# Kernel tuning notes

Measured on AMD Instinct MI355X. Metric: run time of the kernel, lower is better.

## Reference

```python
import jax, jax.numpy as jnp
import numpy as np


def setup_inputs() -> dict:
    key = jax.random.key(0)
    k1, k2, k3, k4, k5 = jax.random.split(key, 5)
    return {
        "d1": jax.random.normal(k1, (2, 4096, 512), dtype=jnp.float32),
        "d2": jax.random.normal(k2, (2, 512, 4096), dtype=jnp.float32),
        "d3": jax.random.normal(k3, (2, 4096, 512), dtype=jnp.float32),
        "d4": jax.random.normal(k4, (512, 512), dtype=jnp.float32),
        "d5": jax.random.normal(k5, (1, 512), dtype=jnp.float32),
    }


def reference(d1, d2, d3, d4, d5):
    # attention core: scores = d1 @ d2 -> [2, 4096, 4096]
    scores = jnp.einsum('bsd,bdt->bst', d1, d2)
    attn = jax.nn.softmax(scores, axis=2)
    # weighted values: [2, 4096, 512]
    ctx = jnp.einsum('bst,btd->bsd', attn, d3)
    # flatten batch*seq and apply final projection with bias (addmm)
    x = ctx.reshape(8192, 512)
    return d5 + x @ d4  # d5 [1,512] broadcasts over rows
```

## Files before the change

### kernel.cpp

```cpp
#include <hip/hip_runtime.h>

typedef unsigned short u16;
typedef __attribute__((ext_vector_type(8))) short short8;
typedef __attribute__((ext_vector_type(4))) float f32x4;

#define MFMA16(a, b, c) __builtin_amdgcn_mfma_f32_16x16x32_bf16((a), (b), (c), 0, 0, 0)

constexpr int Bb = 2, Ss = 4096, Tt = 4096, Dd = 512;
constexpr int BM = 64, BN = 64, TP = 4;
constexpr int TPART = Tt / TP;
constexpr int TCH = TPART / BN;

constexpr size_t SZ_BF = (size_t)Bb * Ss * Dd * 2;
constexpr size_t O_QH  = 0;
constexpr size_t O_QL  = O_QH + SZ_BF;
constexpr size_t O_D2TH = O_QL + SZ_BF;
constexpr size_t O_D2TL = O_D2TH + SZ_BF;
constexpr size_t O_D3T  = O_D2TL + SZ_BF;
constexpr size_t O_D4T  = O_D3T + SZ_BF;
constexpr size_t O_CTX  = O_D4T + (size_t)512 * 512 * 2;
constexpr size_t O_OP   = O_CTX + SZ_BF;
constexpr size_t O_MP   = O_OP + (size_t)TP * SZ_BF;
constexpr size_t O_LP   = O_MP + (size_t)TP * Bb * Ss * 4;

__device__ __forceinline__ u16 f2bf(float x) {
  union { float f; unsigned u; } v; v.f = x;
  unsigned r = v.u + 0x7fffu + ((v.u >> 16) & 1u);
  return (u16)(r >> 16);
}
__device__ __forceinline__ float bf2f(u16 h) {
  union { unsigned u; float f; } v; v.u = ((unsigned)h) << 16;
  return v.f;
}

__device__ __forceinline__ void gl_lds16(const u16* g, u16* l) {
  __builtin_amdgcn_global_load_lds((const __attribute__((address_space(1))) void*)g,
                                   (__attribute__((address_space(3))) void*)l, 16, 0, 0);
}

__global__ void cvt_split_kernel(const float* __restrict__ in,
                                 u16* __restrict__ outh, u16* __restrict__ outl) {
  const int i = blockIdx.x * 256 + threadIdx.x;
  float4 v = ((const float4*)in)[i];
  ushort4 hh, ll;
  hh.x = f2bf(v.x); ll.x = f2bf(v.x - bf2f(hh.x));
  hh.y = f2bf(v.y); ll.y = f2bf(v.y - bf2f(hh.y));
  hh.z = f2bf(v.z); ll.z = f2bf(v.z - bf2f(hh.z));
  hh.w = f2bf(v.w); ll.w = f2bf(v.w - bf2f(hh.w));
  ((ushort4*)outh)[i] = hh;
  ((ushort4*)outl)[i] = ll;
}

__global__ void transpose_split_kernel(const float* __restrict__ in,
                                       u16* __restrict__ outh,
                                       u16* __restrict__ outl,
                                       int R, int C) {
  __shared__ float tile[32][33];
  int b = blockIdx.z;
  const float* inb = in + (size_t)b * R * C;
  int x = blockIdx.x * 32 + threadIdx.x;
  int y0 = blockIdx.y * 32;
  for (int j = threadIdx.y; j < 32; j += 8)
    tile[j][threadIdx.x] = inb[(size_t)(y0 + j) * C + x];
  __syncthreads();
  size_t ob = (size_t)b * C * R;
  for (int j = threadIdx.y; j < 32; j += 8) {
    float v = tile[threadIdx.x][j];
    size_t oi = ob + (size_t)(blockIdx.x * 32 + j) * R + (y0 + threadIdx.x);
    u16 h = f2bf(v);
    outh[oi] = h;
    if (outl) outl[oi] = f2bf(v - bf2f(h));
  }
}

__global__ __launch_bounds__(256, 3)
void flash_part_kernel(const u16* __restrict__ qh_g,
                       const u16* __restrict__ ql_g,
                       const u16* __restrict__ d2th,
                       const u16* __restrict__ d2tl,
                       const u16* __restrict__ d3t,
                       u16* __restrict__ opart,
                       float* __restrict__ mpart,
                       float* __restrict__ lpart) {
  __shared__ __align__(1024) u16 sbuf[2][8192];
  __shared__ __align__(16) u16 ph[64 * 72];

  const int tid = threadIdx.x;
  const int wave = tid >> 6, lane = tid & 63, quad = lane >> 4, l15 = lane & 15;
  const int m0 = wave * 16;
  const int s0 = blockIdx.x * BM, tp = blockIdx.y, b = blockIdx.z;
  const int rr = lane >> 3, sl = lane & 7;
  const int x7 = l15 & 7;

  f32x4 o_acc[32];
#pragma unroll
  for (int i = 0; i < 32; i++) o_acc[i] = (f32x4){0.f, 0.f, 0.f, 0.f};
  float m_r[4] = {-INFINITY, -INFINITY, -INFINITY, -INFINITY};
  float l_r[4] = {0.f, 0.f, 0.f, 0.f};

  const u16* qh_row = qh_g + ((size_t)b * Ss + s0 + m0 + l15) * Dd + quad * 8;
  const u16* ql_row = ql_g + ((size_t)b * Ss + s0 + m0 + l15) * Dd + quad * 8;
  const u16* kh_b = d2th + (size_t)b * Tt * Dd;
  const u16* kl_b = d2tl + (size_t)b * Tt * Dd;
  const u16* v_b  = d3t  + (size_t)b * Dd * Tt;

  short8 qh_r[16], ql_r[16];
#pragma unroll
  for (int t = 0; t < 16; t++) {
    qh_r[t] = *(const short8*)(qh_row + t * 32);
    ql_r[t] = *(const short8*)(ql_row + t * 32);
  }

  auto issueK = [&](int t0, int d0, int bp) {
#pragma unroll
    for (int i = 0; i < 2; i++) {
      const int r0 = wave * 16 + i * 8;
      const int r = r0 + rr;
      const size_t so = (size_t)(t0 + r) * Dd + d0 + ((sl ^ rr) << 3);
      gl_lds16(kh_b + so, &sbuf[bp][r0 * 64]);
      gl_lds16(kl_b + so, &sbuf[bp][4096 + r0 * 64]);
    }
  };
  auto issueV = [&](int t0, int nc, int bp) {
#pragma unroll
    for (int i = 0; i < 4; i++) {
      const int r0 = wave * 32 + i * 8;
      const int r = r0 + rr;
      gl_lds16(v_b + (size_t)(nc * 128 + r) * Tt + t0 + ((sl ^ rr) << 3),
               &sbuf[bp][r0 * 64]);
    }
  };

  issueK(tp * TPART, 0, 0);
  __syncthreads();

  for (int tc = 0; tc < TCH; tc++) {
    const int t0 = tp * TPART + tc * BN;
    f32x4 s_acc[4];
#pragma unroll
    for (int nt = 0; nt < 4; nt++) s_acc[nt] = (f32x4){0.f, 0.f, 0.f, 0.f};

#pragma unroll
    for (int u = 0; u < 8; u++) {
      if (u < 7) issueK(t0, (u + 1) * 64, (u + 1) & 1);
      else       issueV(t0, 0, (u + 1) & 1);
      __builtin_amdgcn_s_setprio(1);
#pragma unroll
      for (int ks = 0; ks < 2; ks++) {
        const int t = u * 2 + ks;
        const int g = ks * 4 + quad;
#pragma unroll
        for (int nt = 0; nt < 4; nt++) {
          const int off = (nt * 16 + l15) * 64 + ((g ^ x7) << 3);
          short8 bh = *(const short8*)&sbuf[u & 1][off];
          short8 bl = *(const short8*)&sbuf[u & 1][4096 + off];
          s_acc[nt] = MFMA16(qh_r[t], bh, s_acc[nt]);
          s_acc[nt] = MFMA16(ql_r[t], bh, s_acc[nt]);
          s_acc[nt] = MFMA16(qh_r[t], bl, s_acc[nt]);
        }
      }
      __builtin_amdgcn_s_setprio(0);
      __syncthreads();
    }

    float alpha[4], psum[4];
#pragma unroll
    for (int r = 0; r < 4; r++) {
      float v = fmaxf(fmaxf(s_acc[0][r], s_acc[1][r]), fmaxf(s_acc[2][r], s_acc[3][r]));
      v = fmaxf(v, __shfl_xor(v, 1));
      v = fmaxf(v, __shfl_xor(v, 2));
      v = fmaxf(v, __shfl_xor(v, 4));
      v = fmaxf(v, __shfl_xor(v, 8));
      float mn = fmaxf(m_r[r], v);
      alpha[r] = __expf(m_r[r] - mn);
      m_r[r] = mn;
      psum[r] = 0.f;
    }
#pragma unroll
    for (int nt = 0; nt < 4; nt++) {
#pragma unroll
      for (int r = 0; r < 4; r++) {
        float p = __expf(s_acc[nt][r] - m_r[r]);
        psum[r] += p;
        ph[(m0 + quad * 4 + r) * 72 + nt * 16 + l15] = f2bf(p);
      }
    }
#pragma unroll
    for (int r = 0; r < 4; r++) {
      float v = psum[r];
      v += __shfl_xor(v, 1);
      v += __shfl_xor(v, 2);
      v += __shfl_xor(v, 4);
      v += __shfl_xor(v, 8);
      l_r[r] = l_r[r] * alpha[r] + v;
    }
#pragma unroll
    for (int j = 0; j < 32; j++) {
#pragma unroll
      for (int r = 0; r < 4; r++) o_acc[j][r] *= alpha[r];
    }

#pragma unroll
    for (int nc = 0; nc < 4; nc++) {
      const int u = 8 + nc;
      if (nc < 3) issueV(t0, nc + 1, (u + 1) & 1);
      else {
        const int tcn = (tc + 1 < TCH) ? tc + 1 : 0;
        issueK(tp * TPART + tcn * BN, 0, (u + 1) & 1);
      }
      __builtin_amdgcn_s_setprio(1);
#pragma unroll
      for (int ks = 0; ks < 2; ks++) {
        const int kk = ks * 32 + quad * 8;
        const int g = ks * 4 + quad;
        short8 ap = *(const short8*)&ph[(m0 + l15) * 72 + kk];
#pragma unroll
        for (int nt = 0; nt < 8; nt++) {
          const int off = (nt * 16 + l15) * 64 + ((g ^ x7) << 3);
          short8 bv = *(const short8*)&sbuf[u & 1][off];
          o_acc[nc * 8 + nt] = MFMA16(ap, bv, o_acc[nc * 8 + nt]);
        }
      }
      __builtin_amdgcn_s_setprio(0);
      __syncthreads();
    }
  }

  const size_t obase = (((size_t)tp * Bb + b) * Ss + s0) * Dd;
#pragma unroll
  for (int j = 0; j < 32; j++) {
    const int col = (j >> 3) * 128 + (j & 7) * 16 + l15;
#pragma unroll
    for (int r = 0; r < 4; r++) {
      const int row = m0 + quad * 4 + r;
      opart[obase + (size_t)row * Dd + col] = f2bf(o_acc[j][r]);
    }
  }
  if (l15 == 0) {
    const size_t sbase = ((size_t)tp * Bb + b) * Ss + s0;
#pragma unroll
    for (int r = 0; r < 4; r++) {
      const int row = m0 + quad * 4 + r;
      mpart[sbase + row] = m_r[r];
      lpart[sbase + row] = l_r[r];
    }
  }
}

__global__ void combine_kernel(const u16* __restrict__ opart,
                               const float* __restrict__ mpart,
                               const float* __restrict__ lpart,
                               u16* __restrict__ ctx) {
  const int idx = blockIdx.x * blockDim.x + threadIdx.x;
  const int vpr = Dd / 8;
  const int row = idx / vpr;
  const int dv = (idx % vpr) * 8;
  float mv[TP], mM = -INFINITY;
#pragma unroll
  for (int p = 0; p < TP; p++) {
    mv[p] = mpart[(size_t)p * Bb * Ss + row];
    mM = fmaxf(mM, mv[p]);
  }
  float w[TP], denom = 0.f;
#pragma unroll
  for (int p = 0; p < TP; p++) {
    float e = __expf(mv[p] - mM);
    w[p] = e;
    denom += e * lpart[(size_t)p * Bb * Ss + row];
  }
  const float inv = 1.0f / denom;
  float acc[8];
#pragma unroll
  for (int e = 0; e < 8; e++) acc[e] = 0.f;
#pragma unroll
  for (int p = 0; p < TP; p++) {
    uint4 raw = *(const uint4*)&opart[(size_t)p * Bb * Ss * Dd + (size_t)row * Dd + dv];
    const u16* u = (const u16*)&raw;
#pragma unroll
    for (int e = 0; e < 8; e++) acc[e] += w[p] * bf2f(u[e]);
  }
  u16 outv[8];
#pragma unroll
  for (int e = 0; e < 8; e++) outv[e] = f2bf(acc[e] * inv);
  *(uint4*)&ctx[(size_t)row * Dd + dv] = *(const uint4*)outv;
}

__global__ __launch_bounds__(256, 2)
void proj_kernel(const u16* __restrict__ ctx,
                 const u16* __restrict__ d4t,
                 const float* __restrict__ d5,
                 float* __restrict__ out) {
  __shared__ u16 a_lds[128 * 40], b_lds[128 * 40];
  const int tid = threadIdx.x;
  const int wave = tid >> 6, lane = tid & 63, quad = lane >> 4, l15 = lane & 15;
  const int m0w = (wave & 1) * 64, n0w = (wave >> 1) * 64;
  const int bm = blockIdx.x, bn = blockIdx.y;
  f32x4 acc[4][4];
#pragma unroll
  for (int i = 0; i < 4; i++)
#pragma unroll
    for (int j = 0; j < 4; j++) acc[i][j] = (f32x4){0.f, 0.f, 0.f, 0.f};

  const int srow = tid >> 2, scol = (tid & 3) * 8;
  for (int kt = 0; kt < 16; kt++) {
    const int k0 = kt * 32;
    __syncthreads();
#pragma unroll
    for (int pass = 0; pass < 2; pass++) {
      const int row = srow + pass * 64;
      *(uint4*)&a_lds[row * 40 + scol] =
          *(const uint4*)&ctx[(size_t)(bm * 128 + row) * Dd + k0 + scol];
      *(uint4*)&b_lds[row * 40 + scol] =
          *(const uint4*)&d4t[(size_t)(bn * 128 + row) * Dd + k0 + scol];
    }
    __syncthreads();
    short8 af[4], bfr[4];
#pragma unroll
    for (int i = 0; i < 4; i++)
      af[i] = *(const short8*)&a_lds[(m0w + 16 * i + l15) * 40 + quad * 8];
#pragma unroll
    for (int j = 0; j < 4; j++)
      bfr[j] = *(const short8*)&b_lds[(n0w + 16 * j + l15) * 40 + quad * 8];
#pragma unroll
    for (int i = 0; i < 4; i++)
#pragma unroll
      for (int j = 0; j < 4; j++) acc[i][j] = MFMA16(af[i], bfr[j], acc[i][j]);
  }
#pragma unroll
  for (int j = 0; j < 4; j++) {
    const int colg = bn * 128 + n0w + 16 * j + l15;
    const float bias = d5[colg];
#pragma unroll
    for (int i = 0; i < 4; i++) {
#pragma unroll
      for (int r = 0; r < 4; r++) {
        const int rowg = bm * 128 + m0w + 16 * i + quad * 4 + r;
        out[(size_t)rowg * 512 + colg] = acc[i][j][r] + bias;
      }
    }
  }
}

extern "C" void kernel_launch(void* const* d_in, const int* in_sizes, int n_in,
                              void* d_out, int out_size, void* d_ws, size_t ws_size,
                              hipStream_t stream) {
  (void)in_sizes; (void)n_in; (void)out_size; (void)ws_size;
  const float* d1 = (const float*)d_in[0];
  const float* d2 = (const float*)d_in[1];
  const float* d3 = (const float*)d_in[2];
  const float* d4 = (const float*)d_in[3];
  const float* d5 = (const float*)d_in[4];
  float* out = (float*)d_out;
  char* ws = (char*)d_ws;

  u16* qh_g = (u16*)(ws + O_QH);
  u16* ql_g = (u16*)(ws + O_QL);
  u16* d2th = (u16*)(ws + O_D2TH);
  u16* d2tl = (u16*)(ws + O_D2TL);
  u16* d3t  = (u16*)(ws + O_D3T);
  u16* d4t  = (u16*)(ws + O_D4T);
  u16* ctx  = (u16*)(ws + O_CTX);
  u16* opart = (u16*)(ws + O_OP);
  float* mpart = (float*)(ws + O_MP);
  float* lpart = (float*)(ws + O_LP);

  cvt_split_kernel<<<(Bb * Ss * Dd / 4) / 256, 256, 0, stream>>>(d1, qh_g, ql_g);
  transpose_split_kernel<<<dim3(128, 16, 2), dim3(32, 8), 0, stream>>>(d2, d2th, d2tl, 512, 4096);
  transpose_split_kernel<<<dim3(16, 128, 2), dim3(32, 8), 0, stream>>>(d3, d3t, nullptr, 4096, 512);
  transpose_split_kernel<<<dim3(16, 16, 1), dim3(32, 8), 0, stream>>>(d4, d4t, nullptr, 512, 512);

  flash_part_kernel<<<dim3(Ss / BM, TP, Bb), 256, 0, stream>>>(qh_g, ql_g, d2th, d2tl, d3t,
                                                               opart, mpart, lpart);
  combine_kernel<<<(Bb * Ss * Dd / 8) / 256, 256, 0, stream>>>(opart, mpart, lpart, ctx);
  proj_kernel<<<dim3(64, 4), 256, 0, stream>>>(ctx, d4t, d5, out);
}
```

Before: 626.2 us.

## Deepen flash kernel pipeline to 4 LDS stages and stream Q from global

Widens the K/V LDS ring from two to four buffers and prefetches three stages ahead, with explicit vmcnt waits and raw barriers in place of __syncthreads. Q hi/lo fragments are no longer held as 32 resident registers but are streamed per stage into a 3-slot register ring using inline-asm global loads. Occupancy is reduced from 3 to 2 blocks per SIMD to make room for the larger LDS footprint. The hand-counted vmcnt values and mixed asm and builtin loads are fragile, and Q is now re-read from global on every T chunk.

New measurement: 705.6 us. 12.7% more time.

```diff
diff --git a/kernel.cpp b/kernel.cpp
--- a/kernel.cpp
+++ b/kernel.cpp
@@ -36,6 +36,10 @@
 __device__ __forceinline__ void gl_lds16(const u16* g, u16* l) {
   __builtin_amdgcn_global_load_lds((const __attribute__((address_space(1))) void*)g,
                                    (__attribute__((address_space(3))) void*)l, 16, 0, 0);
+}
+
+__device__ __forceinline__ void gload_b128(short8& dst, const u16* p) {
+  asm volatile("global_load_dwordx4 %0, %1, off" : "=v"(dst) : "v"(p) : "memory");
 }
 
 __global__ void cvt_split_kernel(const float* __restrict__ in,
@@ -73,7 +77,7 @@
   }
 }
 
-__global__ __launch_bounds__(256, 3)
+__global__ __launch_bounds__(256, 2)
 void flash_part_kernel(const u16* __restrict__ qh_g,
                        const u16* __restrict__ ql_g,
                        const u16* __restrict__ d2th,
@@ -82,7 +86,7 @@
                        u16* __restrict__ opart,
                        float* __restrict__ mpart,
                        float* __restrict__ lpart) {
-  __shared__ __align__(1024) u16 sbuf[2][8192];
+  __shared__ __align__(1024) u16 sbuf[4][8192];
   __shared__ __align__(16) u16 ph[64 * 72];
 
   const int tid = threadIdx.x;
@@ -104,127 +108,145 @@
   const u16* kl_b = d2tl + (size_t)b * Tt * Dd;
   const u16* v_b  = d3t  + (size_t)b * Dd * Tt;
 
-  short8 qh_r[16], ql_r[16];
-#pragma unroll
-  for (int t = 0; t < 16; t++) {
-    qh_r[t] = *(const short8*)(qh_row + t * 32);
-    ql_r[t] = *(const short8*)(ql_row + t * 32);
-  }
-
-  auto issueK = [&](int t0, int d0, int bp) {
+  short8 qh_s[3][2], ql_s[3][2];
+
+  auto issueK = [&](int t0_, int d0_, int bp) {
 #pragma unroll
     for (int i = 0; i < 2; i++) {
       const int r0 = wave * 16 + i * 8;
       const int r = r0 + rr;
-      const size_t so = (size_t)(t0 + r) * Dd + d0 + ((sl ^ rr) << 3);
+      const size_t so = (size_t)(t0_ + r) * Dd + d0_ + ((sl ^ rr) << 3);
       gl_lds16(kh_b + so, &sbuf[bp][r0 * 64]);
       gl_lds16(kl_b + so, &sbuf[bp][4096 + r0 * 64]);
     }
   };
-  auto issueV = [&](int t0, int nc, int bp) {
+  auto issueV = [&](int t0_, int nc, int bp) {
 #pragma unroll
     for (int i = 0; i < 4; i++) {
       const int r0 = wave * 32 + i * 8;
       const int r = r0 + rr;
-      gl_lds16(v_b + (size_t)(nc * 128 + r) * Tt + t0 + ((sl ^ rr) << 3),
+      gl_lds16(v_b + (size_t)(nc * 128 + r) * Tt + t0_ + ((sl ^ rr) << 3),
                &sbuf[bp][r0 * 64]);
     }
   };
-
-  issueK(tp * TPART, 0, 0);
-  __syncthreads();
+  auto issueQ = [&](int uq, int slot) {
+    gload_b128(qh_s[slot][0], qh_row + (2 * uq) * 32);
+    gload_b128(qh_s[slot][1], qh_row + (2 * uq + 1) * 32);
+    gload_b128(ql_s[slot][0], ql_row + (2 * uq) * 32);
+    gload_b128(ql_s[slot][1], ql_row + (2 * uq + 1) * 32);
+  };
+
+  constexpr int VMW[12] = {12, 12, 12, 12, 12, 12, 12, 8, 8, 8, 8, 12};
+
+  const int t00 = tp * TPART;
+  issueK(t00, 0, 0);
+  issueQ(0, 0);
+  issueK(t00, 64, 1);
+  issueQ(1, 1);
+  issueK(t00, 128, 2);
 
   for (int tc = 0; tc < TCH; tc++) {
-    const int t0 = tp * TPART + tc * BN;
+    const int t0 = t00 + tc * BN;
+    const int tcn = (tc + 1 < TCH) ? tc + 1 : 0;
+    const int t0n = t00 + tcn * BN;
     f32x4 s_acc[4];
 #pragma unroll
     for (int nt = 0; nt < 4; nt++) s_acc[nt] = (f32x4){0.f, 0.f, 0.f, 0.f};
 
 #pragma unroll
-    for (int u = 0; u < 8; u++) {
-      if (u < 7) issueK(t0, (u + 1) * 64, (u + 1) & 1);
-      else       issueV(t0, 0, (u + 1) & 1);
-      __builtin_amdgcn_s_setprio(1);
-#pragma unroll
-      for (int ks = 0; ks < 2; ks++) {
-        const int t = u * 2 + ks;
-        const int g = ks * 4 + quad;
+    for (int u = 0; u < 12; u++) {
+      if (u == 8) {
+        float alpha[4], psum[4];
+#pragma unroll
+        for (int r = 0; r < 4; r++) {
+          float v = fmaxf(fmaxf(s_acc[0][r], s_acc[1][r]), fmaxf(s_acc[2][r], s_acc[3][r]));
+          v = fmaxf(v, __shfl_xor(v, 1));
+          v = fmaxf(v, __shfl_xor(v, 2));
+          v = fmaxf(v, __shfl_xor(v, 4));
+          v = fmaxf(v, __shfl_xor(v, 8));
+          float mn = fmaxf(m_r[r], v);
+          alpha[r] = __expf(m_r[r] - mn);
+          m_r[r] = mn;
+          psum[r] = 0.f;
+        }
 #pragma unroll
         for (int nt = 0; nt < 4; nt++) {
-          const int off = (nt * 16 + l15) * 64 + ((g ^ x7) << 3);
-          short8 bh = *(const short8*)&sbuf[u & 1][off];
-          short8 bl = *(const short8*)&sbuf[u & 1][4096 + off];
-          s_acc[nt] = MFMA16(qh_r[t], bh, s_acc[nt]);
-          s_acc[nt] = MFMA16(ql_r[t], bh, s_acc[nt]);
-          s_acc[nt] = MFMA16(qh_r[t], bl, s_acc[nt]);
+#pragma unroll
+          for (int r = 0; r < 4; r++) {
+            float p = __expf(s_acc[nt][r] - m_r[r]);
+            psum[r] += p;
+            ph[(m0 + quad * 4 + r) * 72 + nt * 16 + l15] = f2bf(p);
+          }
+        }
+#pragma unroll
+        for (int r = 0; r < 4; r++) {
+          float v = psum[r];
+          v += __shfl_xor(v, 1);
+          v += __shfl_xor(v, 2);
+          v += __shfl_xor(v, 4);
+          v += __shfl_xor(v, 8);
+          l_r[r] = l_r[r] * alpha[r] + v;
+        }
+#pragma unroll
+        for (int j = 0; j < 32; j++) {
+#pragma unroll
+          for (int r = 0; r < 4; r++) o_acc[j][r] *= alpha[r];
         }
       }
-      __builtin_amdgcn_s_setprio(0);
-      __syncthreads();
-    }
-
-    float alpha[4], psum[4];
-#pragma unroll
-    for (int r = 0; r < 4; r++) {
-      float v = fmaxf(fmaxf(s_acc[0][r], s_acc[1][r]), fmaxf(s_acc[2][r], s_acc[3][r]));
-      v = fmaxf(v, __shfl_xor(v, 1));
-      v = fmaxf(v, __shfl_xor(v, 2));
-      v = fmaxf(v, __shfl_xor(v, 4));
-      v = fmaxf(v, __shfl_xor(v, 8));
-      float mn = fmaxf(m_r[r], v);
-      alpha[r] = __expf(m_r[r] - mn);
-      m_r[r] = mn;
-      psum[r] = 0.f;
-    }
-#pragma unroll
-    for (int nt = 0; nt < 4; nt++) {
-#pragma unroll
-      for (int r = 0; r < 4; r++) {
-        float p = __expf(s_acc[nt][r] - m_r[r]);
-        psum[r] += p;
-        ph[(m0 + quad * 4 + r) * 72 + nt * 16 + l15] = f2bf(p);
+
+      asm volatile("s_waitcnt vmcnt(%0) lgkmcnt(0)" :: "i"(VMW[u]) : "memory");
+      __builtin_amdgcn_s_barrier();
+      __builtin_amdgcn_sched_barrier(0);
+
+      if (u <= 5) {
+        issueQ(u + 2, (u + 2) % 3);
+        if (u < 5) issueK(t0, (u + 3) * 64, (u + 3) & 3);
+        else       issueV(t0, 0, 0);
+      } else if (u == 6)  issueV(t0, 1, 1);
+      else if (u == 7)    issueV(t0, 2, 2);
+      else if (u == 8)    issueV(t0, 3, 3);
+      else if (u == 9)    issueK(t0n, 0, 0);
+      else if (u == 10) { issueQ(0, 0); issueK(t0n, 64, 1); }
+      else              { issueQ(1, 1); issueK(t0n, 128, 2); }
+      __builtin_amdgcn_sched_barrier(0);
+
+      if (u < 8) {
+        __builtin_amdgcn_s_setprio(1);
+#pragma unroll
+        for (int ks = 0; ks < 2; ks++) {
+          const int go = ((ks * 4 + quad) ^ x7) << 3;
+#pragma unroll
+          for (int nt = 0; nt < 4; nt++) {
+            const int off = (nt * 16 + l15) * 64 + go;
+            short8 bh = *(const short8*)&sbuf[u & 3][off];
+            short8 bl = *(const short8*)&sbuf[u & 3][4096 + off];
+            s_acc[nt] = MFMA16(qh_s[u % 3][ks], bh, s_acc[nt]);
+            s_acc[nt] = MFMA16(ql_s[u % 3][ks], bh, s_acc[nt]);
+            s_acc[nt] = MFMA16(qh_s[u % 3][ks], bl, s_acc[nt]);
+          }
+        }
+        __builtin_amdgcn_s_setprio(0);
+      } else {
+        const int nc = u - 8;
+        __builtin_amdgcn_s_setprio(1);
+#pragma unroll
+        for (int ks = 0; ks < 2; ks++) {
+          const int kk = ks * 32 + quad * 8;
+          const int go = ((ks * 4 + quad) ^ x7) << 3;
+          short8 ap = *(const short8*)&ph[(m0 + l15) * 72 + kk];
+#pragma unroll
+          for (int nt = 0; nt < 8; nt++) {
+            const int off = (nt * 16 + l15) * 64 + go;
+            short8 bv = *(const short8*)&sbuf[u & 3][off];
+            o_acc[nc * 8 + nt] = MFMA16(ap, bv, o_acc[nc * 8 + nt]);
+          }
+        }
+        __builtin_amdgcn_s_setprio(0);
       }
     }
-#pragma unroll
-    for (int r = 0; r < 4; r++) {
-      float v = psum[r];
-      v += __shfl_xor(v, 1);
-      v += __shfl_xor(v, 2);
-      v += __shfl_xor(v, 4);
-      v += __shfl_xor(v, 8);
-      l_r[r] = l_r[r] * alpha[r] + v;
-    }
-#pragma unroll
-    for (int j = 0; j < 32; j++) {
-#pragma unroll
-      for (int r = 0; r < 4; r++) o_acc[j][r] *= alpha[r];
-    }
-
-#pragma unroll
-    for (int nc = 0; nc < 4; nc++) {
-      const int u = 8 + nc;
-      if (nc < 3) issueV(t0, nc + 1, (u + 1) & 1);
-      else {
-        const int tcn = (tc + 1 < TCH) ? tc + 1 : 0;
-        issueK(tp * TPART + tcn * BN, 0, (u + 1) & 1);
-      }
-      __builtin_amdgcn_s_setprio(1);
-#pragma unroll
-      for (int ks = 0; ks < 2; ks++) {
-        const int kk = ks * 32 + quad * 8;
-        const int g = ks * 4 + quad;
-        short8 ap = *(const short8*)&ph[(m0 + l15) * 72 + kk];
-#pragma unroll
-        for (int nt = 0; nt < 8; nt++) {
-          const int off = (nt * 16 + l15) * 64 + ((g ^ x7) << 3);
-          short8 bv = *(const short8*)&sbuf[u & 1][off];
-          o_acc[nc * 8 + nt] = MFMA16(ap, bv, o_acc[nc * 8 + nt]);
-        }
-      }
-      __builtin_amdgcn_s_setprio(0);
-      __syncthreads();
-    }
-  }
+  }
+
+  asm volatile("s_waitcnt vmcnt(0)" ::: "memory");
 
   const size_t obase = (((size_t)tp * Bb + b) * Ss + s0) * Dd;
 #pragma unroll
```
